# Performance work log

Measured on AMD Instinct MI355X. Metric: run time of the kernel, lower is better.

The kernel has to match this reference:

```python
import jax, jax.numpy as jnp
import numpy as np

T, IN, H, OUT = 8192, 1024, 1024, 1024

def setup_inputs() -> dict:
    key = jax.random.key(0)
    k1, k2, k3, k4, k5 = jax.random.split(key, 5)
    s_w = 1.0 / np.sqrt(IN + H)
    s_o = 1.0 / np.sqrt(H)
    return {
        "x": jax.random.normal(k1, (T, 1, IN), dtype=jnp.float32),
        "W_w": jax.random.uniform(k2, (4 * H, IN + H), jnp.float32, -s_w, s_w),
        "W_b": jax.random.uniform(k3, (4 * H,), jnp.float32, -s_w, s_w),
        "out_w": jax.random.uniform(k4, (OUT, H), jnp.float32, -s_o, s_o),
        "out_b": jax.random.uniform(k5, (OUT,), jnp.float32, -s_o, s_o),
    }

def reference(x, W_w, W_b, out_w, out_b):
    # x: [T, 1, IN]; gates weight W_w: [4H, IN+H] (torch Linear layout)
    hidden = W_b.shape[0] // 4

    def step(carry, x_t):
        h, c = carry                                   # [1, H] each
        combined = jnp.concatenate([x_t, h], axis=1)   # [1, IN+H]
        gates = combined @ W_w.T + W_b                 # [1, 4H]
        i_t, f_t, g_t, o_t = jnp.split(gates, 4, axis=1)
        c = jax.nn.sigmoid(f_t) * c + jax.nn.sigmoid(i_t) * jnp.tanh(g_t)
        h = jax.nn.sigmoid(o_t) * jnp.tanh(c)
        y = h @ out_w.T + out_b                        # [1, OUT]
        return (h, c), y

    h0 = jnp.zeros((1, hidden), dtype=x.dtype)
    c0 = jnp.zeros((1, hidden), dtype=x.dtype)
    _, ys = jax.lax.scan(step, (h0, c0), x)            # ys: [T, 1, OUT]
    return ys
```

## Files before the change

### kernel.cpp

```cpp
#include <hip/hip_runtime.h>
#include <cstdint>
#include <cstddef>

#define T_STEPS 8192
#define IN_DIM  1024
#define HID     1024
#define OUT_DIM 1024
#define G4      4096

#define NBLK 256
#define TPB  256
#define UPB  4

typedef __attribute__((ext_vector_type(4))) float f32x4;

#define PLOAD(p) __hip_atomic_load((p), __ATOMIC_RELAXED, __HIP_MEMORY_SCOPE_AGENT)

__device__ __forceinline__ float sigf(float x) {
  return 1.0f / (1.0f + __expf(-x));
}

template<int CTRL>
__device__ __forceinline__ float dpp_add(float v) {
  int p = __builtin_amdgcn_update_dpp(0, __float_as_int(v), CTRL, 0xf, 0xf, true);
  return v + __int_as_float(p);
}

__device__ __forceinline__ float wave_sum63(float v) {
  v = dpp_add<0xB1>(v);
  v = dpp_add<0x4E>(v);
  v = dpp_add<0x141>(v);
  v = dpp_add<0x140>(v);
  v = dpp_add<0x142>(v);
  v = dpp_add<0x143>(v);
  return v;
}

__global__ __launch_bounds__(TPB, 1) void lstm_fused(
    const float* __restrict__ Ww,
    const float* __restrict__ xg,
    const float* __restrict__ owm,
    const float* __restrict__ wb,
    const float* __restrict__ obv,
    unsigned long long* __restrict__ hbuf,
    float* __restrict__ out)
{
  __shared__ float whlds[16][HID];
  __shared__ float wxlds[16][HID];
  __shared__ float lh[2][HID];

  const int tid = threadIdx.x;
  const int lane = tid & 63;
  const int wslot = tid >> 6;
  const int u = blockIdx.x * UPB + wslot;

  {
    const float4* __restrict__ Ww4 = (const float4*)Ww;
    float4* wh4 = (float4*)&whlds[0][0];
    float4* wx4 = (float4*)&wxlds[0][0];
    for (int i = tid; i < 16 * 256; i += TPB) {
      const int m = i >> 8;
      const int e4 = i & 255;
      const int gg = m & 3;
      const int ul = m >> 2;
      const size_t row = (size_t)(gg * HID + blockIdx.x * UPB + ul) * 512;
      wh4[i] = Ww4[row + (IN_DIM / 4) + e4];
      wx4[i] = Ww4[row + e4];
    }
  }
  __syncthreads();

  const f32x4* wl4 = (const f32x4*)&whlds[wslot * 4][0];
  const f32x4* wxl = (const f32x4*)&wxlds[wslot * 4][0];

  f32x4 W[16];
#pragma unroll
  for (int r = 0; r < 4; ++r)
#pragma unroll
    for (int k = 0; k < 4; ++k)
      W[r * 4 + k] = wl4[r * 256 + k * 64 + lane];
#pragma unroll
  for (int i = 0; i < 16; ++i) asm volatile("" : "+v"(W[i]));

  f32x4 O[4];
  {
    const f32x4* ow4 = (const f32x4*)(owm + (size_t)u * HID);
#pragma unroll
    for (int k = 0; k < 4; ++k) O[k] = ow4[k * 64 + lane];
#pragma unroll
    for (int k = 0; k < 4; ++k) asm volatile("" : "+v"(O[k]));
  }

  const float bi = wb[u],           bf = wb[HID + u];
  const float bg = wb[2 * HID + u], bo = wb[3 * HID + u];
  const float oby = obv[u];

  float pp[4];
  {
    const f32x4* xt4 = (const f32x4*)xg;
    f32x4 x0[4];
#pragma unroll
    for (int k = 0; k < 4; ++k) x0[k] = xt4[k * 64 + lane];
#pragma unroll
    for (int r = 0; r < 4; ++r) {
      float s = 0.0f;
#pragma unroll
      for (int k = 0; k < 4; ++k) {
        const f32x4 wx = wxl[r * 256 + k * 64 + lane];
        s = fmaf(wx.x, x0[k].x, s); s = fmaf(wx.y, x0[k].y, s);
        s = fmaf(wx.z, x0[k].z, s); s = fmaf(wx.w, x0[k].w, s);
      }
      pp[r] = s;
    }
  }
  f32x4 xnP[4];
  {
    const f32x4* xt4 = (const f32x4*)(xg + (size_t)1 * IN_DIM);
#pragma unroll
    for (int k = 0; k < 4; ++k) xnP[k] = xt4[k * 64 + lane];
  }

  float c = 0.0f;

  for (int t = 0; t <= T_STEPS; ++t) {
    const unsigned long long* hs = hbuf + (size_t)(t & 1) * HID + wslot * 256;
    const unsigned want = (unsigned)t;
    unsigned long long p0, p1, p2, p3;
    for (;;) {
      p0 = PLOAD(hs + lane);
      p1 = PLOAD(hs + 64 + lane);
      p2 = PLOAD(hs + 128 + lane);
      p3 = PLOAD(hs + 192 + lane);
      bool ok = ((unsigned)p0 == want) & ((unsigned)p1 == want) &
                ((unsigned)p2 == want) & ((unsigned)p3 == want);
      if (__all((int)ok)) break;
    }
    {
      float* dst = &lh[t & 1][wslot * 256];
      dst[lane]       = __uint_as_float((unsigned)(p0 >> 32));
      dst[64 + lane]  = __uint_as_float((unsigned)(p1 >> 32));
      dst[128 + lane] = __uint_as_float((unsigned)(p2 >> 32));
      dst[192 + lane] = __uint_as_float((unsigned)(p3 >> 32));
    }

    asm volatile("s_waitcnt lgkmcnt(0)\n\ts_barrier" ::: "memory");

    const f32x4* lhp = (const f32x4*)&lh[t & 1][0];
    f32x4 hv[4];
#pragma unroll
    for (int k = 0; k < 4; ++k) hv[k] = lhp[k * 64 + lane];

    if (t < T_STEPS) {
      float a[4];
#pragma unroll
      for (int r = 0; r < 4; ++r) {
        float s = pp[r];
#pragma unroll
        for (int k = 0; k < 4; ++k) {
          s = fmaf(W[r*4+k].x, hv[k].x, s); s = fmaf(W[r*4+k].y, hv[k].y, s);
          s = fmaf(W[r*4+k].z, hv[k].z, s); s = fmaf(W[r*4+k].w, hv[k].w, s);
        }
        a[r] = wave_sum63(s);
      }
      const float gi = a[0] + bi, gf = a[1] + bf, gc = a[2] + bg, go = a[3] + bo;
      const float si = sigf(gi), sf = sigf(gf), so = sigf(go);
      const float tg = fmaf(2.0f, sigf(2.0f * gc), -1.0f);
      c = fmaf(sf, c, si * tg);
      const float h = so * fmaf(2.0f, sigf(2.0f * c), -1.0f);
      if (lane == 63) {
        const unsigned long long pk =
            ((unsigned long long)__float_as_uint(h) << 32) | (unsigned)(t + 1);
        __hip_atomic_store(hbuf + (size_t)((t + 1) & 1) * HID + u, pk,
                           __ATOMIC_RELAXED, __HIP_MEMORY_SCOPE_AGENT);
      }
    }

    __builtin_amdgcn_sched_barrier(0);

    f32x4 xnN[4];
    const bool pf = (t + 2 < T_STEPS);
    if (pf) {
      const f32x4* xt4 = (const f32x4*)(xg + (size_t)(t + 2) * IN_DIM);
#pragma unroll
      for (int k = 0; k < 4; ++k) xnN[k] = xt4[k * 64 + lane];
    }

    if (t > 0) {
      float yv = 0.0f;
#pragma unroll
      for (int k = 0; k < 4; ++k) {
        yv = fmaf(O[k].x, hv[k].x, yv); yv = fmaf(O[k].y, hv[k].y, yv);
        yv = fmaf(O[k].z, hv[k].z, yv); yv = fmaf(O[k].w, hv[k].w, yv);
      }
      yv = wave_sum63(yv);
      if (lane == 63) out[(size_t)(t - 1) * OUT_DIM + u] = yv + oby;
    }
    __builtin_amdgcn_sched_barrier(0);

    if (t + 1 < T_STEPS) {
#pragma unroll
      for (int r = 0; r < 4; ++r) {
        float s = 0.0f;
#pragma unroll
        for (int k = 0; k < 4; ++k) {
          const f32x4 wx = wxl[r * 256 + k * 64 + lane];
          s = fmaf(wx.x, xnP[k].x, s); s = fmaf(wx.y, xnP[k].y, s);
          s = fmaf(wx.z, xnP[k].z, s); s = fmaf(wx.w, xnP[k].w, s);
        }
        pp[r] = s;
      }
    }

    if (pf) {
#pragma unroll
      for (int k = 0; k < 4; ++k) xnP[k] = xnN[k];
    }
  }
}

extern "C" void kernel_launch(void* const* d_in, const int* in_sizes, int n_in,
                              void* d_out, int out_size, void* d_ws, size_t ws_size,
                              hipStream_t stream) {
  (void)in_sizes; (void)n_in; (void)out_size; (void)ws_size;

  const float* x     = (const float*)d_in[0];
  const float* W_w   = (const float*)d_in[1];
  const float* W_b   = (const float*)d_in[2];
  const float* out_w = (const float*)d_in[3];
  const float* out_b = (const float*)d_in[4];
  float* out = (float*)d_out;

  unsigned long long* hbuf = (unsigned long long*)d_ws;
  hipMemsetAsync(d_ws, 0, 16384, stream);

  lstm_fused<<<NBLK, TPB, 0, stream>>>(W_w, x, out_w, W_b, out_b, hbuf, out);
}
```

Baseline: 11.63 ms.

## Halve block count with two hidden units per wave to shrink sync fan-in

Each wave now computes two hidden units instead of one, so the grid drops from 256 to 128 blocks and fewer workgroups take part in the per-step global handshake. Recurrent weights are loaded straight from global memory into registers, doubling the register-resident weights. The input-projection weights stay in LDS, which doubles to 32 rows. The aim is lower cross-block synchronisation and polling overhead per timestep. The cost is twice the serial work per wave on the critical path, plus higher VGPR and LDS pressure.

```diff
diff --git a/kernel.cpp b/kernel.cpp
--- a/kernel.cpp
+++ b/kernel.cpp
@@ -6,11 +6,11 @@
 #define IN_DIM  1024
 #define HID     1024
 #define OUT_DIM 1024
-#define G4      4096
-
-#define NBLK 256
+
+#define NBLK 128
 #define TPB  256
-#define UPB  4
+#define UPB  8
+#define UPW  2
 
 typedef __attribute__((ext_vector_type(4))) float f32x4;
 
@@ -45,72 +45,86 @@
     unsigned long long* __restrict__ hbuf,
     float* __restrict__ out)
 {
-  __shared__ float whlds[16][HID];
-  __shared__ float wxlds[16][HID];
+  __shared__ float wxlds[32][HID];
   __shared__ float lh[2][HID];
 
   const int tid = threadIdx.x;
   const int lane = tid & 63;
   const int wslot = tid >> 6;
-  const int u = blockIdx.x * UPB + wslot;
+  const int u0 = blockIdx.x * UPB + wslot * UPW;
 
   {
     const float4* __restrict__ Ww4 = (const float4*)Ww;
-    float4* wh4 = (float4*)&whlds[0][0];
     float4* wx4 = (float4*)&wxlds[0][0];
-    for (int i = tid; i < 16 * 256; i += TPB) {
+    for (int i = tid; i < 32 * 256; i += TPB) {
       const int m = i >> 8;
       const int e4 = i & 255;
       const int gg = m & 3;
       const int ul = m >> 2;
       const size_t row = (size_t)(gg * HID + blockIdx.x * UPB + ul) * 512;
-      wh4[i] = Ww4[row + (IN_DIM / 4) + e4];
       wx4[i] = Ww4[row + e4];
     }
   }
+
+  f32x4 W[32];
+  {
+    const f32x4* WwG = (const f32x4*)Ww;
+#pragma unroll
+    for (int q = 0; q < UPW; ++q)
+#pragma unroll
+      for (int r = 0; r < 4; ++r)
+#pragma unroll
+        for (int k = 0; k < 4; ++k)
+          W[(q * 4 + r) * 4 + k] =
+              WwG[(size_t)(r * HID + u0 + q) * 512 + 256 + k * 64 + lane];
+#pragma unroll
+    for (int i = 0; i < 16; ++i) asm volatile("" : "+v"(W[i]));
+#pragma unroll
+    for (int i = 16; i < 32; ++i) asm volatile("" : "+v"(W[i]));
+  }
+
+  f32x4 O[8];
+  {
+#pragma unroll
+    for (int q = 0; q < UPW; ++q) {
+      const f32x4* ow4 = (const f32x4*)(owm + (size_t)(u0 + q) * HID);
+#pragma unroll
+      for (int k = 0; k < 4; ++k) O[q * 4 + k] = ow4[k * 64 + lane];
+    }
+#pragma unroll
+    for (int i = 0; i < 8; ++i) asm volatile("" : "+v"(O[i]));
+  }
+
+  float bi[UPW], bf[UPW], bg[UPW], bo[UPW], oby[UPW];
+#pragma unroll
+  for (int q = 0; q < UPW; ++q) {
+    bi[q] = wb[u0 + q];           bf[q] = wb[HID + u0 + q];
+    bg[q] = wb[2 * HID + u0 + q]; bo[q] = wb[3 * HID + u0 + q];
+    oby[q] = obv[u0 + q];
+  }
+
   __syncthreads();
 
-  const f32x4* wl4 = (const f32x4*)&whlds[wslot * 4][0];
-  const f32x4* wxl = (const f32x4*)&wxlds[wslot * 4][0];
-
-  f32x4 W[16];
-#pragma unroll
-  for (int r = 0; r < 4; ++r)
-#pragma unroll
-    for (int k = 0; k < 4; ++k)
-      W[r * 4 + k] = wl4[r * 256 + k * 64 + lane];
-#pragma unroll
-  for (int i = 0; i < 16; ++i) asm volatile("" : "+v"(W[i]));
-
-  f32x4 O[4];
-  {
-    const f32x4* ow4 = (const f32x4*)(owm + (size_t)u * HID);
-#pragma unroll
-    for (int k = 0; k < 4; ++k) O[k] = ow4[k * 64 + lane];
-#pragma unroll
-    for (int k = 0; k < 4; ++k) asm volatile("" : "+v"(O[k]));
-  }
-
-  const float bi = wb[u],           bf = wb[HID + u];
-  const float bg = wb[2 * HID + u], bo = wb[3 * HID + u];
-  const float oby = obv[u];
-
-  float pp[4];
+  float pp[8];
   {
     const f32x4* xt4 = (const f32x4*)xg;
     f32x4 x0[4];
 #pragma unroll
     for (int k = 0; k < 4; ++k) x0[k] = xt4[k * 64 + lane];
 #pragma unroll
-    for (int r = 0; r < 4; ++r) {
-      float s = 0.0f;
-#pragma unroll
-      for (int k = 0; k < 4; ++k) {
-        const f32x4 wx = wxl[r * 256 + k * 64 + lane];
-        s = fmaf(wx.x, x0[k].x, s); s = fmaf(wx.y, x0[k].y, s);
-        s = fmaf(wx.z, x0[k].z, s); s = fmaf(wx.w, x0[k].w, s);
-      }
-      pp[r] = s;
+    for (int q = 0; q < UPW; ++q) {
+      const f32x4* wxl = (const f32x4*)&wxlds[(wslot * UPW + q) * 4][0];
+#pragma unroll
+      for (int r = 0; r < 4; ++r) {
+        float s = 0.0f;
+#pragma unroll
+        for (int k = 0; k < 4; ++k) {
+          const f32x4 wx = wxl[r * 256 + k * 64 + lane];
+          s = fmaf(wx.x, x0[k].x, s); s = fmaf(wx.y, x0[k].y, s);
+          s = fmaf(wx.z, x0[k].z, s); s = fmaf(wx.w, x0[k].w, s);
+        }
+        pp[q * 4 + r] = s;
+      }
     }
   }
   f32x4 xnP[4];
@@ -120,7 +134,9 @@
     for (int k = 0; k < 4; ++k) xnP[k] = xt4[k * 64 + lane];
   }
 
-  float c = 0.0f;
+  float cs[UPW];
+#pragma unroll
+  for (int q = 0; q < UPW; ++q) cs[q] = 0.0f;
 
   for (int t = 0; t <= T_STEPS; ++t) {
     const unsigned long long* hs = hbuf + (size_t)(t & 1) * HID + wslot * 256;
@@ -151,27 +167,34 @@
     for (int k = 0; k < 4; ++k) hv[k] = lhp[k * 64 + lane];
 
     if (t < T_STEPS) {
-      float a[4];
-#pragma unroll
-      for (int r = 0; r < 4; ++r) {
-        float s = pp[r];
-#pragma unroll
-        for (int k = 0; k < 4; ++k) {
-          s = fmaf(W[r*4+k].x, hv[k].x, s); s = fmaf(W[r*4+k].y, hv[k].y, s);
-          s = fmaf(W[r*4+k].z, hv[k].z, s); s = fmaf(W[r*4+k].w, hv[k].w, s);
-        }
-        a[r] = wave_sum63(s);
-      }
-      const float gi = a[0] + bi, gf = a[1] + bf, gc = a[2] + bg, go = a[3] + bo;
-      const float si = sigf(gi), sf = sigf(gf), so = sigf(go);
-      const float tg = fmaf(2.0f, sigf(2.0f * gc), -1.0f);
-      c = fmaf(sf, c, si * tg);
-      const float h = so * fmaf(2.0f, sigf(2.0f * c), -1.0f);
-      if (lane == 63) {
-        const unsigned long long pk =
-            ((unsigned long long)__float_as_uint(h) << 32) | (unsigned)(t + 1);
-        __hip_atomic_store(hbuf + (size_t)((t + 1) & 1) * HID + u, pk,
-                           __ATOMIC_RELAXED, __HIP_MEMORY_SCOPE_AGENT);
+      float a[8];
+#pragma unroll
+      for (int q = 0; q < UPW; ++q)
+#pragma unroll
+        for (int r = 0; r < 4; ++r) {
+          float s = pp[q * 4 + r];
+          const int w0 = (q * 4 + r) * 4;
+#pragma unroll
+          for (int k = 0; k < 4; ++k) {
+            s = fmaf(W[w0+k].x, hv[k].x, s); s = fmaf(W[w0+k].y, hv[k].y, s);
+            s = fmaf(W[w0+k].z, hv[k].z, s); s = fmaf(W[w0+k].w, hv[k].w, s);
+          }
+          a[q * 4 + r] = wave_sum63(s);
+        }
+#pragma unroll
+      for (int q = 0; q < UPW; ++q) {
+        const float gi = a[q*4+0] + bi[q], gf = a[q*4+1] + bf[q];
+        const float gc = a[q*4+2] + bg[q], go = a[q*4+3] + bo[q];
+        const float si = sigf(gi), sf = sigf(gf), so = sigf(go);
+        const float tg = fmaf(2.0f, sigf(2.0f * gc), -1.0f);
+        cs[q] = fmaf(sf, cs[q], si * tg);
+        const float h = so * fmaf(2.0f, sigf(2.0f * cs[q]), -1.0f);
+        if (lane == 63) {
+          const unsigned long long pk =
+              ((unsigned long long)__float_as_uint(h) << 32) | (unsigned)(t + 1);
+          __hip_atomic_store(hbuf + (size_t)((t + 1) & 1) * HID + u0 + q, pk,
+                             __ATOMIC_RELAXED, __HIP_MEMORY_SCOPE_AGENT);
+        }
       }
     }
 
@@ -186,28 +209,35 @@
     }
 
     if (t > 0) {
-      float yv = 0.0f;
-#pragma unroll
-      for (int k = 0; k < 4; ++k) {
-        yv = fmaf(O[k].x, hv[k].x, yv); yv = fmaf(O[k].y, hv[k].y, yv);
-        yv = fmaf(O[k].z, hv[k].z, yv); yv = fmaf(O[k].w, hv[k].w, yv);
-      }
-      yv = wave_sum63(yv);
-      if (lane == 63) out[(size_t)(t - 1) * OUT_DIM + u] = yv + oby;
+#pragma unroll
+      for (int q = 0; q < UPW; ++q) {
+        float yv = 0.0f;
+#pragma unroll
+        for (int k = 0; k < 4; ++k) {
+          yv = fmaf(O[q*4+k].x, hv[k].x, yv); yv = fmaf(O[q*4+k].y, hv[k].y, yv);
+          yv = fmaf(O[q*4+k].z, hv[k].z, yv); yv = fmaf(O[q*4+k].w, hv[k].w, yv);
+        }
+        yv = wave_sum63(yv);
+        if (lane == 63) out[(size_t)(t - 1) * OUT_DIM + u0 + q] = yv + oby[q];
+      }
     }
     __builtin_amdgcn_sched_barrier(0);
 
     if (t + 1 < T_STEPS) {
 #pragma unroll
-      for (int r = 0; r < 4; ++r) {
-        float s = 0.0f;
-#pragma unroll
-        for (int k = 0; k < 4; ++k) {
-          const f32x4 wx = wxl[r * 256 + k * 64 + lane];
-          s = fmaf(wx.x, xnP[k].x, s); s = fmaf(wx.y, xnP[k].y, s);
-          s = fmaf(wx.z, xnP[k].z, s); s = fmaf(wx.w, xnP[k].w, s);
-        }
-        pp[r] = s;
+      for (int q = 0; q < UPW; ++q) {
+        const f32x4* wxl = (const f32x4*)&wxlds[(wslot * UPW + q) * 4][0];
+#pragma unroll
+        for (int r = 0; r < 4; ++r) {
+          float s = 0.0f;
+#pragma unroll
+          for (int k = 0; k < 4; ++k) {
+            const f32x4 wx = wxl[r * 256 + k * 64 + lane];
+            s = fmaf(wx.x, xnP[k].x, s); s = fmaf(wx.y, xnP[k].y, s);
+            s = fmaf(wx.z, xnP[k].z, s); s = fmaf(wx.w, xnP[k].w, s);
+          }
+          pp[q * 4 + r] = s;
+        }
       }
     }
 
```

Result: slower. 15.93 ms (+37.0%).

## Offload input projection and output head to a dedicated helper wave per block

Applied to the files above, without the earlier changes.

Adds a fifth wave per block that computes all four units' output projections and the next step's x·Wx partial sums, passing the partials to the four recurrent waves through a double-buffered LDS array. The recurrent waves now only poll h, do the h·Wh dot products and the gate math, which shortens the serial critical path of each timestep. The cost is more register pressure on the helper wave (16 output vectors) and a dependency on the shared per-step barrier. The helper wave inserts an s_sleep, and x loads are no longer prefetched, so it could fall behind and stall the barrier.

```diff
diff --git a/kernel.cpp b/kernel.cpp
--- a/kernel.cpp
+++ b/kernel.cpp
@@ -6,10 +6,9 @@
 #define IN_DIM  1024
 #define HID     1024
 #define OUT_DIM 1024
-#define G4      4096
 
 #define NBLK 256
-#define TPB  256
+#define TPB  320
 #define UPB  4
 
 typedef __attribute__((ext_vector_type(4))) float f32x4;
@@ -48,11 +47,12 @@
   __shared__ float whlds[16][HID];
   __shared__ float wxlds[16][HID];
   __shared__ float lh[2][HID];
+  __shared__ float pplds[2][16][64];
 
   const int tid = threadIdx.x;
   const int lane = tid & 63;
   const int wslot = tid >> 6;
-  const int u = blockIdx.x * UPB + wslot;
+  const int ub = blockIdx.x * UPB;
 
   {
     const float4* __restrict__ Ww4 = (const float4*)Ww;
@@ -63,157 +63,164 @@
       const int e4 = i & 255;
       const int gg = m & 3;
       const int ul = m >> 2;
-      const size_t row = (size_t)(gg * HID + blockIdx.x * UPB + ul) * 512;
+      const size_t row = (size_t)(gg * HID + ub + ul) * 512;
       wh4[i] = Ww4[row + (IN_DIM / 4) + e4];
       wx4[i] = Ww4[row + e4];
     }
   }
   __syncthreads();
 
-  const f32x4* wl4 = (const f32x4*)&whlds[wslot * 4][0];
-  const f32x4* wxl = (const f32x4*)&wxlds[wslot * 4][0];
-
-  f32x4 W[16];
-#pragma unroll
-  for (int r = 0; r < 4; ++r)
-#pragma unroll
-    for (int k = 0; k < 4; ++k)
-      W[r * 4 + k] = wl4[r * 256 + k * 64 + lane];
-#pragma unroll
-  for (int i = 0; i < 16; ++i) asm volatile("" : "+v"(W[i]));
-
-  f32x4 O[4];
-  {
-    const f32x4* ow4 = (const f32x4*)(owm + (size_t)u * HID);
-#pragma unroll
-    for (int k = 0; k < 4; ++k) O[k] = ow4[k * 64 + lane];
-#pragma unroll
-    for (int k = 0; k < 4; ++k) asm volatile("" : "+v"(O[k]));
-  }
-
-  const float bi = wb[u],           bf = wb[HID + u];
-  const float bg = wb[2 * HID + u], bo = wb[3 * HID + u];
-  const float oby = obv[u];
-
-  float pp[4];
-  {
-    const f32x4* xt4 = (const f32x4*)xg;
-    f32x4 x0[4];
-#pragma unroll
-    for (int k = 0; k < 4; ++k) x0[k] = xt4[k * 64 + lane];
-#pragma unroll
-    for (int r = 0; r < 4; ++r) {
-      float s = 0.0f;
-#pragma unroll
-      for (int k = 0; k < 4; ++k) {
-        const f32x4 wx = wxl[r * 256 + k * 64 + lane];
-        s = fmaf(wx.x, x0[k].x, s); s = fmaf(wx.y, x0[k].y, s);
-        s = fmaf(wx.z, x0[k].z, s); s = fmaf(wx.w, x0[k].w, s);
-      }
-      pp[r] = s;
-    }
-  }
-  f32x4 xnP[4];
-  {
-    const f32x4* xt4 = (const f32x4*)(xg + (size_t)1 * IN_DIM);
-#pragma unroll
-    for (int k = 0; k < 4; ++k) xnP[k] = xt4[k * 64 + lane];
-  }
-
-  float c = 0.0f;
-
-  for (int t = 0; t <= T_STEPS; ++t) {
-    const unsigned long long* hs = hbuf + (size_t)(t & 1) * HID + wslot * 256;
-    const unsigned want = (unsigned)t;
-    unsigned long long p0, p1, p2, p3;
-    for (;;) {
-      p0 = PLOAD(hs + lane);
-      p1 = PLOAD(hs + 64 + lane);
-      p2 = PLOAD(hs + 128 + lane);
-      p3 = PLOAD(hs + 192 + lane);
-      bool ok = ((unsigned)p0 == want) & ((unsigned)p1 == want) &
-                ((unsigned)p2 == want) & ((unsigned)p3 == want);
-      if (__all((int)ok)) break;
-    }
+  if (wslot < UPB) {
+    const int u = ub + wslot;
+    const f32x4* wl4 = (const f32x4*)&whlds[wslot * 4][0];
+
+    f32x4 W[16];
+#pragma unroll
+    for (int r = 0; r < 4; ++r)
+#pragma unroll
+      for (int k = 0; k < 4; ++k)
+        W[r * 4 + k] = wl4[r * 256 + k * 64 + lane];
+#pragma unroll
+    for (int i = 0; i < 16; ++i) asm volatile("" : "+v"(W[i]));
+
+    const float bi = wb[u],           bf = wb[HID + u];
+    const float bg = wb[2 * HID + u], bo = wb[3 * HID + u];
+
+    __syncthreads();
+
+    float c = 0.0f;
+
+    for (int t = 0; t <= T_STEPS; ++t) {
+      const unsigned long long* hs = hbuf + (size_t)(t & 1) * HID + wslot * 256;
+      const unsigned want = (unsigned)t;
+      unsigned long long p0, p1, p2, p3;
+      for (;;) {
+        p0 = PLOAD(hs + lane);
+        p1 = PLOAD(hs + 64 + lane);
+        p2 = PLOAD(hs + 128 + lane);
+        p3 = PLOAD(hs + 192 + lane);
+        bool ok = ((unsigned)p0 == want) & ((unsigned)p1 == want) &
+                  ((unsigned)p2 == want) & ((unsigned)p3 == want);
+        if (__all((int)ok)) break;
+      }
+      {
+        float* dst = &lh[t & 1][wslot * 256];
+        dst[lane]       = __uint_as_float((unsigned)(p0 >> 32));
+        dst[64 + lane]  = __uint_as_float((unsigned)(p1 >> 32));
+        dst[128 + lane] = __uint_as_float((unsigned)(p2 >> 32));
+        dst[192 + lane] = __uint_as_float((unsigned)(p3 >> 32));
+      }
+
+      asm volatile("s_waitcnt lgkmcnt(0)\n\ts_barrier" ::: "memory");
+
+      const f32x4* lhp = (const f32x4*)&lh[t & 1][0];
+      f32x4 hv[4];
+#pragma unroll
+      for (int k = 0; k < 4; ++k) hv[k] = lhp[k * 64 + lane];
+
+      if (t < T_STEPS) {
+        const float* ppb = &pplds[t & 1][wslot * 4][0];
+        float a[4];
+#pragma unroll
+        for (int r = 0; r < 4; ++r) {
+          float s = ppb[r * 64 + lane];
+#pragma unroll
+          for (int k = 0; k < 4; ++k) {
+            s = fmaf(W[r*4+k].x, hv[k].x, s); s = fmaf(W[r*4+k].y, hv[k].y, s);
+            s = fmaf(W[r*4+k].z, hv[k].z, s); s = fmaf(W[r*4+k].w, hv[k].w, s);
+          }
+          a[r] = wave_sum63(s);
+        }
+        const float gi = a[0] + bi, gf = a[1] + bf, gc = a[2] + bg, go = a[3] + bo;
+        const float si = sigf(gi), sf = sigf(gf), so = sigf(go);
+        const float tg = fmaf(2.0f, sigf(2.0f * gc), -1.0f);
+        c = fmaf(sf, c, si * tg);
+        const float h = so * fmaf(2.0f, sigf(2.0f * c), -1.0f);
+        if (lane == 63) {
+          const unsigned long long pk =
+              ((unsigned long long)__float_as_uint(h) << 32) | (unsigned)(t + 1);
+          __hip_atomic_store(hbuf + (size_t)((t + 1) & 1) * HID + u, pk,
+                             __ATOMIC_RELAXED, __HIP_MEMORY_SCOPE_AGENT);
+        }
+      }
+      __builtin_amdgcn_sched_barrier(0);
+    }
+  } else {
+    f32x4 O[16];
+#pragma unroll
+    for (int q = 0; q < 4; ++q) {
+      const f32x4* ow4 = (const f32x4*)(owm + (size_t)(ub + q) * HID);
+#pragma unroll
+      for (int k = 0; k < 4; ++k) O[q * 4 + k] = ow4[k * 64 + lane];
+    }
+#pragma unroll
+    for (int i = 0; i < 16; ++i) asm volatile("" : "+v"(O[i]));
+
+    float oby[4];
+#pragma unroll
+    for (int q = 0; q < 4; ++q) oby[q] = obv[ub + q];
+
     {
-      float* dst = &lh[t & 1][wslot * 256];
-      dst[lane]       = __uint_as_float((unsigned)(p0 >> 32));
-      dst[64 + lane]  = __uint_as_float((unsigned)(p1 >> 32));
-      dst[128 + lane] = __uint_as_float((unsigned)(p2 >> 32));
-      dst[192 + lane] = __uint_as_float((unsigned)(p3 >> 32));
-    }
-
-    asm volatile("s_waitcnt lgkmcnt(0)\n\ts_barrier" ::: "memory");
-
-    const f32x4* lhp = (const f32x4*)&lh[t & 1][0];
-    f32x4 hv[4];
-#pragma unroll
-    for (int k = 0; k < 4; ++k) hv[k] = lhp[k * 64 + lane];
-
-    if (t < T_STEPS) {
-      float a[4];
-#pragma unroll
-      for (int r = 0; r < 4; ++r) {
-        float s = pp[r];
+      const f32x4* xt4 = (const f32x4*)xg;
+      f32x4 xv[4];
+#pragma unroll
+      for (int k = 0; k < 4; ++k) xv[k] = xt4[k * 64 + lane];
+#pragma unroll
+      for (int m = 0; m < 16; ++m) {
+        const f32x4* wxm = (const f32x4*)&wxlds[m][0];
+        float s = 0.0f;
 #pragma unroll
         for (int k = 0; k < 4; ++k) {
-          s = fmaf(W[r*4+k].x, hv[k].x, s); s = fmaf(W[r*4+k].y, hv[k].y, s);
-          s = fmaf(W[r*4+k].z, hv[k].z, s); s = fmaf(W[r*4+k].w, hv[k].w, s);
-        }
-        a[r] = wave_sum63(s);
-      }
-      const float gi = a[0] + bi, gf = a[1] + bf, gc = a[2] + bg, go = a[3] + bo;
-      const float si = sigf(gi), sf = sigf(gf), so = sigf(go);
-      const float tg = fmaf(2.0f, sigf(2.0f * gc), -1.0f);
-      c = fmaf(sf, c, si * tg);
-      const float h = so * fmaf(2.0f, sigf(2.0f * c), -1.0f);
-      if (lane == 63) {
-        const unsigned long long pk =
-            ((unsigned long long)__float_as_uint(h) << 32) | (unsigned)(t + 1);
-        __hip_atomic_store(hbuf + (size_t)((t + 1) & 1) * HID + u, pk,
-                           __ATOMIC_RELAXED, __HIP_MEMORY_SCOPE_AGENT);
-      }
-    }
-
-    __builtin_amdgcn_sched_barrier(0);
-
-    f32x4 xnN[4];
-    const bool pf = (t + 2 < T_STEPS);
-    if (pf) {
-      const f32x4* xt4 = (const f32x4*)(xg + (size_t)(t + 2) * IN_DIM);
-#pragma unroll
-      for (int k = 0; k < 4; ++k) xnN[k] = xt4[k * 64 + lane];
-    }
-
-    if (t > 0) {
-      float yv = 0.0f;
-#pragma unroll
-      for (int k = 0; k < 4; ++k) {
-        yv = fmaf(O[k].x, hv[k].x, yv); yv = fmaf(O[k].y, hv[k].y, yv);
-        yv = fmaf(O[k].z, hv[k].z, yv); yv = fmaf(O[k].w, hv[k].w, yv);
-      }
-      yv = wave_sum63(yv);
-      if (lane == 63) out[(size_t)(t - 1) * OUT_DIM + u] = yv + oby;
-    }
-    __builtin_amdgcn_sched_barrier(0);
-
-    if (t + 1 < T_STEPS) {
-#pragma unroll
-      for (int r = 0; r < 4; ++r) {
-        float s = 0.0f;
-#pragma unroll
-        for (int k = 0; k < 4; ++k) {
-          const f32x4 wx = wxl[r * 256 + k * 64 + lane];
-          s = fmaf(wx.x, xnP[k].x, s); s = fmaf(wx.y, xnP[k].y, s);
-          s = fmaf(wx.z, xnP[k].z, s); s = fmaf(wx.w, xnP[k].w, s);
-        }
-        pp[r] = s;
-      }
-    }
-
-    if (pf) {
-#pragma unroll
-      for (int k = 0; k < 4; ++k) xnP[k] = xnN[k];
+          const f32x4 wx = wxm[k * 64 + lane];
+          s = fmaf(wx.x, xv[k].x, s); s = fmaf(wx.y, xv[k].y, s);
+          s = fmaf(wx.z, xv[k].z, s); s = fmaf(wx.w, xv[k].w, s);
+        }
+        pplds[0][m][lane] = s;
+      }
+    }
+    __syncthreads();
+
+    for (int t = 0; t <= T_STEPS; ++t) {
+      asm volatile("s_waitcnt lgkmcnt(0)\n\ts_barrier" ::: "memory");
+      asm volatile("s_sleep 8" ::: "memory");
+
+      const f32x4* lhp = (const f32x4*)&lh[t & 1][0];
+      f32x4 hv[4];
+#pragma unroll
+      for (int k = 0; k < 4; ++k) hv[k] = lhp[k * 64 + lane];
+
+      if (t > 0) {
+#pragma unroll
+        for (int q = 0; q < 4; ++q) {
+          float yv = 0.0f;
+#pragma unroll
+          for (int k = 0; k < 4; ++k) {
+            yv = fmaf(O[q*4+k].x, hv[k].x, yv); yv = fmaf(O[q*4+k].y, hv[k].y, yv);
+            yv = fmaf(O[q*4+k].z, hv[k].z, yv); yv = fmaf(O[q*4+k].w, hv[k].w, yv);
+          }
+          yv = wave_sum63(yv);
+          if (lane == 63) out[(size_t)(t - 1) * OUT_DIM + ub + q] = yv + oby[q];
+        }
+      }
+
+      if (t + 1 < T_STEPS) {
+        const f32x4* xt4 = (const f32x4*)(xg + (size_t)(t + 1) * IN_DIM);
+        f32x4 xv[4];
+#pragma unroll
+        for (int k = 0; k < 4; ++k) xv[k] = xt4[k * 64 + lane];
+#pragma unroll
+        for (int m = 0; m < 16; ++m) {
+          const f32x4* wxm = (const f32x4*)&wxlds[m][0];
+          float s = 0.0f;
+#pragma unroll
+          for (int k = 0; k < 4; ++k) {
+            const f32x4 wx = wxm[k * 64 + lane];
+            s = fmaf(wx.x, xv[k].x, s); s = fmaf(wx.y, xv[k].y, s);
+            s = fmaf(wx.z, xv[k].z, s); s = fmaf(wx.w, xv[k].w, s);
+          }
+          pplds[(t + 1) & 1][m][lane] = s;
+        }
+      }
     }
   }
 }
```

After: 30.86 ms. 165% more time.
